# Kernel optimization log

Hardware: AMD Instinct MI355X
Metric: run time of the kernel (lower is better)

The kernel has to match this reference:

```python
import jax, jax.numpy as jnp
import numpy as np

# Module hyperparameters (BNMorph.__init__ defaults + KITTI resolution)
B, H, W = 8, 320, 1024
SEARCH_W = 7      # serachWidth
SEARCH_H = 3      # searchHeight
SPARSITY_RAD = 2
SENSE_R = 20
PIX_DW = 24.0     # pixel_distance_weight
ALPHA_DW = 0.7    # alpha_distance_weight
PIX_MUL_DW = 1.9  # pixel_mulline_distance_weight
ALPHA_PAD = 1.6   # alpha_padding
EDGE_DENSITY = 0.02


def _make_offsets():
    # Exactly mirrors BNMorph.__init__ buffer construction.
    rs = np.arange(-SEARCH_W, SEARCH_W + 1)
    cs = np.arange(-SEARCH_H, SEARCH_H + 1)
    xx, yy = np.meshgrid(rs, cs)
    xx = xx.flatten(); yy = yy.flatten()
    idx = np.argsort(xx ** 2 + yy ** 2)
    xx = xx[idx]; yy = yy[idx]
    ss = np.arange(-SPARSITY_RAD, SPARSITY_RAD + 1)
    sxx, syy = np.meshgrid(ss, ss)
    sxx = sxx.flatten(); syy = syy.flatten()
    cspan = np.arange(-SENSE_R, SENSE_R + 1)
    cxx, cyy = np.meshgrid(cspan, cspan)
    cxx = cxx.flatten(); cyy = cyy.flatten()
    ci = np.argsort(cxx ** 2 + cyy ** 2)
    cxx = cxx[ci]; cyy = cyy[ci]
    f32 = lambda a: jnp.asarray(a, dtype=jnp.float32)
    return f32(xx), f32(yy), f32(sxx), f32(syy), f32(cxx), f32(cyy)


def setup_inputs() -> dict:
    key = jax.random.key(0)
    k1, k2 = jax.random.split(key)
    binMapsrc = (jax.random.uniform(k1, (B, 1, H, W)) < EDGE_DENSITY).astype(jnp.float32)
    binMapdst = (jax.random.uniform(k2, (B, 1, H, W)) < EDGE_DENSITY).astype(jnp.float32)
    xx, yy, sxx, syy, cxx, cyy = _make_offsets()
    return {"binMapsrc": binMapsrc, "binMapdst": binMapdst,
            "xx": xx, "yy": yy, "sxx": sxx, "syy": syy, "cxx": cxx, "cyy": cyy}


def _forward(binMapsrc, binMapdst, xx, yy, sxx, syy, cxx, cyy):
    src = binMapsrc[:, 0] > 0.5  # [B,H,W] bool
    dst = binMapdst[:, 0] > 0.5
    b, h, w = src.shape

    # ---- 1. sparsity filtering of src edge points ----
    # keep an active pixel iff no active pixel precedes it (raster order)
    # inside the sparsity window -> approximates greedy sparsification.
    sdx = sxx.astype(jnp.int32); sdy = syy.astype(jnp.int32)
    prec = ((sdy < 0) | ((sdy == 0) & (sdx < 0))).astype(jnp.float32)
    Ps = jnp.pad(src.astype(jnp.float32),
                 ((0, 0), (SPARSITY_RAD, SPARSITY_RAD), (SPARSITY_RAD, SPARSITY_RAD)))

    def sp_step(acc, off):
        dx, dy, wk = off
        sl = jax.lax.dynamic_slice(Ps, (0, SPARSITY_RAD + dy, SPARSITY_RAD + dx), (b, h, w))
        return acc + sl * wk, None

    acc, _ = jax.lax.scan(sp_step, jnp.zeros((b, h, w), jnp.float32), (sdx, sdy, prec))
    kept = src & (acc < 0.5)

    # ---- 2. windowed nearest-correspondence search in dst ----
    # offsets (xx,yy) are pre-sorted by distance, so the first hit is nearest.
    qdx = xx.astype(jnp.int32); qdy = yy.astype(jnp.int32)
    Pd = jnp.pad(dst, ((0, 0), (SEARCH_H, SEARCH_H), (SEARCH_W, SEARCH_W)))

    def m_step(carry, off):
        found, vx, vy = carry
        dx, dy, dxf, dyf = off
        sl = jax.lax.dynamic_slice(Pd, (0, SEARCH_H + dy, SEARCH_W + dx), (b, h, w))
        hit = sl & kept & (~found)
        vx = jnp.where(hit, dxf, vx)
        vy = jnp.where(hit, dyf, vy)
        return (found | hit, vx, vy), None

    init = (jnp.zeros((b, h, w), bool),
            jnp.zeros((b, h, w), jnp.float32),
            jnp.zeros((b, h, w), jnp.float32))
    (found, vx, vy), _ = jax.lax.scan(m_step, init, (qdx, qdy, xx, yy))

    # ---- 3. distance-weighted morph field (splat = depthwise conv) ----
    d = jnp.sqrt(cxx ** 2 + cyy ** 2)
    wts = ALPHA_DW * jnp.exp(-d * PIX_MUL_DW / PIX_DW)
    R = SENSE_R
    K = jnp.zeros((2 * R + 1, 2 * R + 1), jnp.float32)
    K = K.at[cyy.astype(jnp.int32) + R, cxx.astype(jnp.int32) + R].set(wts)

    m = found.astype(jnp.float32)
    inp = jnp.stack([m, m * vx, m * vy], axis=1)        # [B,3,H,W]
    ker = jnp.tile(K[None, None], (3, 1, 1, 1))          # [3,1,41,41]
    out = jax.lax.conv_general_dilated(
        inp, ker, (1, 1), ((R, R), (R, R)),
        dimension_numbers=("NCHW", "OIHW", "NCHW"), feature_group_count=3)
    den = out[:, 0] + ALPHA_PAD
    dispx = out[:, 1] / den
    dispy = out[:, 2] / den

    ygrid, xgrid = jnp.meshgrid(jnp.arange(h, dtype=jnp.float32),
                                jnp.arange(w, dtype=jnp.float32), indexing="ij")
    morphedx = xgrid + dispx
    morphedy = ygrid + dispy
    orgpts_x = xgrid * m
    orgpts_y = ygrid * m
    correspts_x = (xgrid + vx) * m
    correspts_y = (ygrid + vy) * m
    return morphedx, morphedy, orgpts_x, orgpts_y, correspts_x, correspts_y


def reference(binMapsrc, binMapdst, xx, yy, sxx, syy, cxx, cyy):
    return _forward(binMapsrc, binMapdst, xx, yy, sxx, syy, cxx, cyy)
```

## Files before the change

### kernel.cpp

```cpp
#include <hip/hip_runtime.h>


#define BB 8
#define HH 320
#define WW 1024
#define N_PIX (BB*HH*WW)
#define WPI (HH*(WW/32))
#define RR 20
#define TLW 64
#define TLH 16
#define TXN (WW/TLW)
#define TYN (HH/TLH)
#define NQ 105
#define CAP 160
#define NCR (TLH+40)
#define NSR (NCR+2)
#define NDR (NCR+6)
#define WSTRIDE 49
#define WTABN 2060
#define WTAB_OFF (2*BB*WPI*4)

#define O_WTAB  0
#define O_SRC   8240
#define O_DST   9632
#define O_WAV   8240
#define O_SPT   11120
#define O_PRANK 11792
#define O_SVB   12224
#define O_LCNT  13248
#define SMEM_BYTES 13264

typedef unsigned long long u64;
typedef float v2f __attribute__((ext_vector_type(2)));

__global__ __launch_bounds__(256) void pack_zero(
    const float* __restrict__ src, const float* __restrict__ dst,
    unsigned* __restrict__ packed, float* __restrict__ wtab_g)
{
    int t = threadIdx.x;
    int i = blockIdx.x * 256 + t;
    if (i < WTABN) {
        int row = i / WSTRIDE, c = i - row * WSTRIDE;
        float v = 0.0f;
        if (row <= 40 && c >= 4 && c <= 44) {
            int dxv = c - 24, dyv = row - 20;
            float d = sqrtf((float)(dxv * dxv + dyv * dyv));
            v = 0.7f * expf((-d * 1.9f) / 24.0f);
        }
        wtab_g[i] = v;
    }
    const float4* p = (i < (N_PIX >> 2)) ? (const float4*)src + i
                                         : (const float4*)dst + (i - (N_PIX >> 2));
    float4 v = *p;
    unsigned nib = (v.x > 0.5f ? 1u : 0u) | (v.y > 0.5f ? 2u : 0u)
                 | (v.z > 0.5f ? 4u : 0u) | (v.w > 0.5f ? 8u : 0u);
    unsigned val = nib << ((t & 7) * 4);
    val |= __shfl_xor(val, 1);
    val |= __shfl_xor(val, 2);
    val |= __shfl_xor(val, 4);
    if ((t & 7) == 0) packed[i >> 3] = val;
}

__global__ __launch_bounds__(128, 6) void fused_morph(
    const unsigned* __restrict__ packed,
    const float* __restrict__ xx, const float* __restrict__ yy,
    const float* __restrict__ wtab_g,
    float* __restrict__ out)
{
    __shared__ __align__(16) unsigned char sMem[SMEM_BYTES];
    float* wtab = (float*)(sMem + O_WTAB);
    unsigned (*sSrc)[6] = (unsigned(*)[6])(sMem + O_SRC);
    unsigned (*sDst)[6] = (unsigned(*)[6])(sMem + O_DST);
    unsigned* sPt = (unsigned*)(sMem + O_SPT);
    int* prank = (int*)(sMem + O_PRANK);
    unsigned char* sVB = sMem + O_SVB;
    int* lcnt = (int*)(sMem + O_LCNT);

    int t = threadIdx.x;
    int txT = blockIdx.x, tyT = blockIdx.y, b = blockIdx.z;
    int tx0 = txT * TLW, ty0 = tyT * TLH;
    int wb0 = (tx0 >> 5) - 1;
    const unsigned* psrc = packed + (size_t)b * WPI;
    const unsigned* pdst = packed + (size_t)(BB + b) * WPI;

    for (int i = t; i < WTABN / 4; i += 128)
        ((float4*)wtab)[i] = ((const float4*)wtab_g)[i];
    for (int i = t; i < NSR * 4; i += 128) {
        int r = i >> 2, w = (i & 3) + 1;
        int gy = ty0 - 22 + r, gw = wb0 + (w - 1);
        sSrc[r][w] = (gy >= 0 && gy < HH && gw >= 0 && gw < 32) ? psrc[(gy << 5) + gw] : 0u;
    }
    for (int i = t; i < NDR * 4; i += 128) {
        int r = i >> 2, w = (i & 3) + 1;
        int gy = ty0 - 23 + r, gw = wb0 + (w - 1);
        sDst[r][w] = (gy >= 0 && gy < HH && gw >= 0 && gw < 32) ? pdst[(gy << 5) + gw] : 0u;
    }
    if (t < NDR) { sDst[t][0] = 0; sDst[t][5] = 0; if (t < NSR) { sSrc[t][0] = 0; sSrc[t][5] = 0; } }
    if (t < NQ) {
        int dx = (int)xx[t], dy = (int)yy[t];
        prank[(dy + 3) * 15 + (dx + 7)] = (t << 8) | ((dx + 7) << 4) | (dy + 3);
    }
    ((unsigned*)sVB)[t] = 0; ((unsigned*)sVB)[t + 128] = 0;
    if (t == 0) lcnt[0] = 0;
    __syncthreads();

    for (int task = t; task < NCR * 4; task += 128) {
        int cr = task >> 2, w = (task & 3) + 1;
        unsigned C = sSrc[cr + 2][w];
        unsigned found = 0;
        if (C) {
            #define EXT5(row) ( (u64)((row)[w-1] >> 30) \
                              | ((u64)(row)[w] << 2) \
                              | ((u64)((row)[w+1] & 3u) << 34) )
            u64 a = EXT5(sSrc[cr]) | EXT5(sSrc[cr + 1]);
            u64 or5 = a | (a >> 1) | (a >> 2) | (a >> 3) | (a >> 4);
            u64 e2 = EXT5(sSrc[cr + 2]);
            unsigned kept = C & ~(unsigned)(or5 | e2 | (e2 >> 1));
            if (kept) {
                u64 dil = 0;
                #pragma unroll
                for (int rr = 0; rr < 7; ++rr) {
                    const unsigned* row = sDst[cr + rr];
                    dil |= (u64)(row[w-1] >> 25) | ((u64)row[w] << 7)
                         | ((u64)(row[w+1] & 0x7Fu) << 39);
                }
                u64 a2 = dil | (dil >> 1);
                u64 b2 = a2 | (a2 >> 2);
                u64 c2 = b2 | (b2 >> 4);
                u64 o15 = c2 | (c2 >> 7);
                found = kept & (unsigned)o15;
            }
        }
        if (w == 1) found &= 0xFFFFF000u;
        if (w == 4) found &= 0x000FFFFFu;
        if (found) {
            int nf = __popc(found);
            int base = atomicAdd(lcnt, nf);
            unsigned fi = found;
            while (fi) {
                int bit = __builtin_ctz(fi); fi &= fi - 1;
                int px = tx0 - 32 + ((w - 1) << 5) + bit;
                if (base < CAP) sPt[base] = (unsigned)((cr << 10) | px);
                ++base;
            }
        }
    }
    __syncthreads();
    int nPts = lcnt[0]; if (nPts > CAP) nPts = CAP;

    for (int i = t; i < nPts; i += 128) {
        unsigned e = sPt[i];
        int cr = (int)(e >> 10), px = (int)(e & 1023u);
        int q = px - tx0 + 25;
        int widx = 1 + (q >> 5), sh = q & 31;
        u64 lo = 0, hi = 0;
        #pragma unroll
        for (int rr = 0; rr < 7; ++rr) {
            const unsigned* row = sDst[cr + rr];
            u64 win = (((u64)row[widx] | ((u64)row[widx + 1] << 32)) >> sh) & 0x7FFFull;
            if (rr < 4) lo |= win << (15 * rr);
            else        hi |= win << (15 * (rr - 4));
        }
        int minv = 0x7FFFFFFF;
        while (lo) { int bb2 = __builtin_ctzll(lo); lo &= lo - 1; int rv = prank[bb2];      if (rv < minv) minv = rv; }
        while (hi) { int bb2 = __builtin_ctzll(hi); hi &= hi - 1; int rv = prank[60 + bb2]; if (rv < minv) minv = rv; }
        int vxp7 = (minv >> 4) & 15, vyp3 = minv & 15;
        int py = ty0 - 20 + cr;
        sPt[i] = (unsigned)px | ((unsigned)py << 10)
               | ((unsigned)vxp7 << 19) | ((unsigned)vyp3 << 23);
        if (px >= tx0 && px < tx0 + TLW && cr >= 20 && cr < 20 + TLH)
            sVB[(cr - 20) * TLW + (px - tx0)] =
                (unsigned char)(0x80 | vxp7 | (vyp3 << 4));
    }
    __syncthreads();

    int lane = t & 63, w = __builtin_amdgcn_readfirstlane(t >> 6);
    unsigned* sWavW = (unsigned*)(sMem + O_WAV) + w * 164;
    int wy0 = ty0 + w * 8;
    int cw = 0;
    for (int base = 0; base < nPts; base += 64) {
        int i = base + lane;
        unsigned pk = (i < nPts) ? sPt[i] : 0xFFFFFFFFu;
        int py = (int)((pk >> 10) & 511u);
        bool pass = (i < nPts) & (py >= wy0 - 20) & (py <= wy0 + 27);
        u64 m = __ballot(pass);
        if (pass) {
            int idx = __popcll(m & ((1ull << lane) - 1ull));
            sWavW[cw + idx] = pk;
        }
        cw += __popcll(m);
    }
    int c4 = (cw + 3) & ~3;
    if (lane < c4 - cw) sWavW[cw + lane] = 0xFFFFFFFFu;

    int x0q = tx0 + (lane & 15) * 4;
    int yg  = wy0 + (lane >> 4);

    v2f a0p[2][2] = {};
    v2f av[2][4]  = {};

    for (int p = 0; p < c4; p += 4) {
        uint4 P = *(const uint4*)&sWavW[p];
        #pragma unroll
        for (int k = 0; k < 4; ++k) {
            int spk = __builtin_amdgcn_readfirstlane(
                (int)(k == 0 ? P.x : k == 1 ? P.y : k == 2 ? P.z : P.w));
            int pxp21 = (spk & 1023) + 21;
            int pyp20 = ((spk >> 10) & 511) + 20;
            float pvx = (float)(((spk >> 19) & 15) - 7);
            float pvy = (float)(((spk >> 23) & 7) - 3);
            v2f vv = {pvx, pvy};

            int coff = pxp21 - x0q;
            coff = coff < 0 ? 0 : (coff > 45 ? 45 : coff);
            int d0r = pyp20 - yg;
            #pragma unroll
            for (int ry = 0; ry < 2; ++ry) {
                int dyr = d0r - 4 * ry;
                int rowi = ((unsigned)dyr > 40u) ? 41 : dyr;
                const float* wr = &wtab[rowi * WSTRIDE + coff];
                float w3 = wr[0], w2 = wr[1], w1 = wr[2], w0 = wr[3];
                a0p[ry][0] += (v2f){w0, w1};
                a0p[ry][1] += (v2f){w2, w3};
                av[ry][0] += w0 * vv;
                av[ry][1] += w1 * vv;
                av[ry][2] += w2 * vv;
                av[ry][3] += w3 * vv;
            }
        }
    }

    size_t bbase = (size_t)b * HH * WW;
    int lx = x0q - tx0;
    #pragma unroll
    for (int ry = 0; ry < 2; ++ry) {
        int y = yg + 4 * ry;
        int ly = y - ty0;
        unsigned vb4 = *(const unsigned*)&sVB[ly * TLW + lx];
        size_t idx = bbase + (size_t)y * WW + x0q;
        float d0 = a0p[ry][0].x + 1.6f, d1 = a0p[ry][0].y + 1.6f;
        float d2 = a0p[ry][1].x + 1.6f, d3 = a0p[ry][1].y + 1.6f;
        float4 ox = { (float)x0q     + av[ry][0].x / d0, (float)(x0q+1) + av[ry][1].x / d1,
                      (float)(x0q+2) + av[ry][2].x / d2, (float)(x0q+3) + av[ry][3].x / d3 };
        float4 oy = { (float)y + av[ry][0].y / d0, (float)y + av[ry][1].y / d1,
                      (float)y + av[ry][2].y / d2, (float)y + av[ry][3].y / d3 };
        float4 o2, o3, o4, o5;
        float* po2 = &o2.x; float* po3 = &o3.x; float* po4 = &o4.x; float* po5 = &o5.x;
        #pragma unroll
        for (int jj = 0; jj < 4; ++jj) {
            unsigned by = (vb4 >> (8 * jj)) & 255u;
            float fm  = (float)(by >> 7);
            float fvx = (float)((int)(by & 15u) - 7);
            float fvy = (float)((int)((by >> 4) & 7u) - 3);
            float fx  = (float)(x0q + jj);
            po2[jj] = fx * fm;
            po3[jj] = (float)y * fm;
            po4[jj] = (fx + fvx) * fm;
            po5[jj] = ((float)y + fvy) * fm;
        }
        *reinterpret_cast<float4*>(out + idx)                     = ox;
        *reinterpret_cast<float4*>(out + (size_t)N_PIX + idx)     = oy;
        *reinterpret_cast<float4*>(out + 2 * (size_t)N_PIX + idx) = o2;
        *reinterpret_cast<float4*>(out + 3 * (size_t)N_PIX + idx) = o3;
        *reinterpret_cast<float4*>(out + 4 * (size_t)N_PIX + idx) = o4;
        *reinterpret_cast<float4*>(out + 5 * (size_t)N_PIX + idx) = o5;
    }
}

extern "C" void kernel_launch(void* const* d_in, const int* in_sizes, int n_in,
                              void* d_out, int out_size, void* d_ws, size_t ws_size,
                              hipStream_t stream) {
    const float* src = (const float*)d_in[0];
    const float* dst = (const float*)d_in[1];
    const float* xx  = (const float*)d_in[2];
    const float* yy  = (const float*)d_in[3];
    float* out = (float*)d_out;

    unsigned* packed = (unsigned*)d_ws;
    float*    wtab_g = (float*)((char*)d_ws + WTAB_OFF);

    pack_zero<<<(2 * N_PIX / 4) / 256, 256, 0, stream>>>(src, dst, packed, wtab_g);

    dim3 g2(TXN, TYN, BB);
    fused_morph<<<g2, 128, 0, stream>>>(packed, xx, yy, wtab_g, out);
}
```

Measured before the change: 127.3 us.

## Shrink fused morph tile width to 32 and give each lane one output row

Halves the tile width from 64 to 32 pixels, so the grid doubles and each lane now accumulates a single output row of four pixels instead of two rows. The bit-packed src/dst halo buffers become 5 words per row with new word indexing, and the shared-memory layout, point capacity and weight-table stride are resized to match. The aim is more blocks and fewer registers per thread for better occupancy and load balance. In exchange, halo loading and sparsification/search work are repeated across more tiles, and each wave must rescan the points in its region for fewer outputs.

```diff
diff --git a/kernel.cpp b/kernel.cpp
--- a/kernel.cpp
+++ b/kernel.cpp
@@ -6,29 +6,28 @@
 #define WW 1024
 #define N_PIX (BB*HH*WW)
 #define WPI (HH*(WW/32))
-#define RR 20
-#define TLW 64
+#define TLW 32
 #define TLH 16
 #define TXN (WW/TLW)
 #define TYN (HH/TLH)
 #define NQ 105
-#define CAP 160
+#define CAP 112
 #define NCR (TLH+40)
 #define NSR (NCR+2)
 #define NDR (NCR+6)
-#define WSTRIDE 49
-#define WTABN 2060
+#define WSTRIDE 53
+#define WTABN 2228
 #define WTAB_OFF (2*BB*WPI*4)
 
 #define O_WTAB  0
-#define O_SRC   8240
-#define O_DST   9632
-#define O_WAV   8240
-#define O_SPT   11120
+#define O_SRC   8912
+#define O_WAV   8912
+#define O_DST   10072
+#define O_SPT   11312
 #define O_PRANK 11792
 #define O_SVB   12224
-#define O_LCNT  13248
-#define SMEM_BYTES 13264
+#define O_LCNT  12736
+#define SMEM_BYTES 12752
 
 typedef unsigned long long u64;
 typedef float v2f __attribute__((ext_vector_type(2)));
@@ -69,8 +68,8 @@
 {
     __shared__ __align__(16) unsigned char sMem[SMEM_BYTES];
     float* wtab = (float*)(sMem + O_WTAB);
-    unsigned (*sSrc)[6] = (unsigned(*)[6])(sMem + O_SRC);
-    unsigned (*sDst)[6] = (unsigned(*)[6])(sMem + O_DST);
+    unsigned (*sSrc)[5] = (unsigned(*)[5])(sMem + O_SRC);
+    unsigned (*sDst)[5] = (unsigned(*)[5])(sMem + O_DST);
     unsigned* sPt = (unsigned*)(sMem + O_SPT);
     int* prank = (int*)(sMem + O_PRANK);
     unsigned char* sVB = sMem + O_SVB;
@@ -79,39 +78,37 @@
     int t = threadIdx.x;
     int txT = blockIdx.x, tyT = blockIdx.y, b = blockIdx.z;
     int tx0 = txT * TLW, ty0 = tyT * TLH;
-    int wb0 = (tx0 >> 5) - 1;
     const unsigned* psrc = packed + (size_t)b * WPI;
     const unsigned* pdst = packed + (size_t)(BB + b) * WPI;
 
     for (int i = t; i < WTABN / 4; i += 128)
         ((float4*)wtab)[i] = ((const float4*)wtab_g)[i];
-    for (int i = t; i < NSR * 4; i += 128) {
-        int r = i >> 2, w = (i & 3) + 1;
-        int gy = ty0 - 22 + r, gw = wb0 + (w - 1);
-        sSrc[r][w] = (gy >= 0 && gy < HH && gw >= 0 && gw < 32) ? psrc[(gy << 5) + gw] : 0u;
-    }
-    for (int i = t; i < NDR * 4; i += 128) {
-        int r = i >> 2, w = (i & 3) + 1;
-        int gy = ty0 - 23 + r, gw = wb0 + (w - 1);
-        sDst[r][w] = (gy >= 0 && gy < HH && gw >= 0 && gw < 32) ? pdst[(gy << 5) + gw] : 0u;
-    }
-    if (t < NDR) { sDst[t][0] = 0; sDst[t][5] = 0; if (t < NSR) { sSrc[t][0] = 0; sSrc[t][5] = 0; } }
+    for (int i = t; i < NSR * 5; i += 128) {
+        int r = i / 5, k = i - r * 5;
+        int gy = ty0 - 22 + r, gw = txT - 2 + k;
+        sSrc[r][k] = (gy >= 0 && gy < HH && gw >= 0 && gw < 32) ? psrc[(gy << 5) + gw] : 0u;
+    }
+    for (int i = t; i < NDR * 5; i += 128) {
+        int r = i / 5, k = i - r * 5;
+        int gy = ty0 - 23 + r, gw = txT - 2 + k;
+        sDst[r][k] = (gy >= 0 && gy < HH && gw >= 0 && gw < 32) ? pdst[(gy << 5) + gw] : 0u;
+    }
     if (t < NQ) {
         int dx = (int)xx[t], dy = (int)yy[t];
         prank[(dy + 3) * 15 + (dx + 7)] = (t << 8) | ((dx + 7) << 4) | (dy + 3);
     }
-    ((unsigned*)sVB)[t] = 0; ((unsigned*)sVB)[t + 128] = 0;
+    ((unsigned*)sVB)[t] = 0;
     if (t == 0) lcnt[0] = 0;
     __syncthreads();
 
-    for (int task = t; task < NCR * 4; task += 128) {
-        int cr = task >> 2, w = (task & 3) + 1;
-        unsigned C = sSrc[cr + 2][w];
+    for (int task = t; task < NCR * 3; task += 128) {
+        int cr = task / 3, wd = task - cr * 3 + 1;
+        unsigned C = sSrc[cr + 2][wd];
         unsigned found = 0;
         if (C) {
-            #define EXT5(row) ( (u64)((row)[w-1] >> 30) \
-                              | ((u64)(row)[w] << 2) \
-                              | ((u64)((row)[w+1] & 3u) << 34) )
+            #define EXT5(row) ( (u64)((row)[wd-1] >> 30) \
+                              | ((u64)(row)[wd] << 2) \
+                              | ((u64)((row)[wd+1] & 3u) << 34) )
             u64 a = EXT5(sSrc[cr]) | EXT5(sSrc[cr + 1]);
             u64 or5 = a | (a >> 1) | (a >> 2) | (a >> 3) | (a >> 4);
             u64 e2 = EXT5(sSrc[cr + 2]);
@@ -121,8 +118,8 @@
                 #pragma unroll
                 for (int rr = 0; rr < 7; ++rr) {
                     const unsigned* row = sDst[cr + rr];
-                    dil |= (u64)(row[w-1] >> 25) | ((u64)row[w] << 7)
-                         | ((u64)(row[w+1] & 0x7Fu) << 39);
+                    dil |= (u64)(row[wd-1] >> 25) | ((u64)row[wd] << 7)
+                         | ((u64)(row[wd+1] & 0x7Fu) << 39);
                 }
                 u64 a2 = dil | (dil >> 1);
                 u64 b2 = a2 | (a2 >> 2);
@@ -131,15 +128,15 @@
                 found = kept & (unsigned)o15;
             }
         }
-        if (w == 1) found &= 0xFFFFF000u;
-        if (w == 4) found &= 0x000FFFFFu;
+        if (wd == 1) found &= 0xFFFFF000u;
+        if (wd == 3) found &= 0x000FFFFFu;
         if (found) {
             int nf = __popc(found);
             int base = atomicAdd(lcnt, nf);
             unsigned fi = found;
             while (fi) {
                 int bit = __builtin_ctz(fi); fi &= fi - 1;
-                int px = tx0 - 32 + ((w - 1) << 5) + bit;
+                int px = tx0 - 64 + (wd << 5) + bit;
                 if (base < CAP) sPt[base] = (unsigned)((cr << 10) | px);
                 ++base;
             }
@@ -151,8 +148,8 @@
     for (int i = t; i < nPts; i += 128) {
         unsigned e = sPt[i];
         int cr = (int)(e >> 10), px = (int)(e & 1023u);
-        int q = px - tx0 + 25;
-        int widx = 1 + (q >> 5), sh = q & 31;
+        int q = px - tx0 + 57;
+        int widx = q >> 5, sh = q & 31;
         u64 lo = 0, hi = 0;
         #pragma unroll
         for (int rr = 0; rr < 7; ++rr) {
@@ -175,7 +172,7 @@
     __syncthreads();
 
     int lane = t & 63, w = __builtin_amdgcn_readfirstlane(t >> 6);
-    unsigned* sWavW = (unsigned*)(sMem + O_WAV) + w * 164;
+    unsigned* sWavW = (unsigned*)(sMem + O_WAV) + w * 120;
     int wy0 = ty0 + w * 8;
     int cw = 0;
     for (int base = 0; base < nPts; base += 64) {
@@ -193,11 +190,11 @@
     int c4 = (cw + 3) & ~3;
     if (lane < c4 - cw) sWavW[cw + lane] = 0xFFFFFFFFu;
 
-    int x0q = tx0 + (lane & 15) * 4;
-    int yg  = wy0 + (lane >> 4);
-
-    v2f a0p[2][2] = {};
-    v2f av[2][4]  = {};
+    int x0q = tx0 + (lane & 7) * 4;
+    int y   = wy0 + (lane >> 3);
+
+    v2f a0p0 = {}, a0p1 = {};
+    v2f av[4] = {};
 
     for (int p = 0; p < c4; p += 4) {
         uint4 P = *(const uint4*)&sWavW[p];
@@ -205,66 +202,56 @@
         for (int k = 0; k < 4; ++k) {
             int spk = __builtin_amdgcn_readfirstlane(
                 (int)(k == 0 ? P.x : k == 1 ? P.y : k == 2 ? P.z : P.w));
-            int pxp21 = (spk & 1023) + 21;
+            int px = spk & 1023;
             int pyp20 = ((spk >> 10) & 511) + 20;
             float pvx = (float)(((spk >> 19) & 15) - 7);
             float pvy = (float)(((spk >> 23) & 7) - 3);
             v2f vv = {pvx, pvy};
 
-            int coff = pxp21 - x0q;
+            int coff = px + 21 - x0q;
             coff = coff < 0 ? 0 : (coff > 45 ? 45 : coff);
-            int d0r = pyp20 - yg;
-            #pragma unroll
-            for (int ry = 0; ry < 2; ++ry) {
-                int dyr = d0r - 4 * ry;
-                int rowi = ((unsigned)dyr > 40u) ? 41 : dyr;
-                const float* wr = &wtab[rowi * WSTRIDE + coff];
-                float w3 = wr[0], w2 = wr[1], w1 = wr[2], w0 = wr[3];
-                a0p[ry][0] += (v2f){w0, w1};
-                a0p[ry][1] += (v2f){w2, w3};
-                av[ry][0] += w0 * vv;
-                av[ry][1] += w1 * vv;
-                av[ry][2] += w2 * vv;
-                av[ry][3] += w3 * vv;
-            }
+            int dyr = pyp20 - y;
+            int rowi = ((unsigned)dyr > 40u) ? 41 : dyr;
+            const float* wr = &wtab[rowi * WSTRIDE + coff];
+            float w3 = wr[0], w2 = wr[1], w1 = wr[2], w0 = wr[3];
+            a0p0 += (v2f){w0, w1};
+            a0p1 += (v2f){w2, w3};
+            av[0] += w0 * vv;
+            av[1] += w1 * vv;
+            av[2] += w2 * vv;
+            av[3] += w3 * vv;
         }
     }
 
     size_t bbase = (size_t)b * HH * WW;
-    int lx = x0q - tx0;
+    unsigned vb4 = *(const unsigned*)&sVB[(y - ty0) * TLW + (x0q - tx0)];
+    size_t idx = bbase + (size_t)y * WW + x0q;
+    float d0 = a0p0.x + 1.6f, d1 = a0p0.y + 1.6f;
+    float d2 = a0p1.x + 1.6f, d3 = a0p1.y + 1.6f;
+    float4 ox = { (float)x0q     + av[0].x / d0, (float)(x0q+1) + av[1].x / d1,
+                  (float)(x0q+2) + av[2].x / d2, (float)(x0q+3) + av[3].x / d3 };
+    float4 oy = { (float)y + av[0].y / d0, (float)y + av[1].y / d1,
+                  (float)y + av[2].y / d2, (float)y + av[3].y / d3 };
+    float4 o2, o3, o4, o5;
+    float* po2 = &o2.x; float* po3 = &o3.x; float* po4 = &o4.x; float* po5 = &o5.x;
     #pragma unroll
-    for (int ry = 0; ry < 2; ++ry) {
-        int y = yg + 4 * ry;
-        int ly = y - ty0;
-        unsigned vb4 = *(const unsigned*)&sVB[ly * TLW + lx];
-        size_t idx = bbase + (size_t)y * WW + x0q;
-        float d0 = a0p[ry][0].x + 1.6f, d1 = a0p[ry][0].y + 1.6f;
-        float d2 = a0p[ry][1].x + 1.6f, d3 = a0p[ry][1].y + 1.6f;
-        float4 ox = { (float)x0q     + av[ry][0].x / d0, (float)(x0q+1) + av[ry][1].x / d1,
-                      (float)(x0q+2) + av[ry][2].x / d2, (float)(x0q+3) + av[ry][3].x / d3 };
-        float4 oy = { (float)y + av[ry][0].y / d0, (float)y + av[ry][1].y / d1,
-                      (float)y + av[ry][2].y / d2, (float)y + av[ry][3].y / d3 };
-        float4 o2, o3, o4, o5;
-        float* po2 = &o2.x; float* po3 = &o3.x; float* po4 = &o4.x; float* po5 = &o5.x;
-        #pragma unroll
-        for (int jj = 0; jj < 4; ++jj) {
-            unsigned by = (vb4 >> (8 * jj)) & 255u;
-            float fm  = (float)(by >> 7);
-            float fvx = (float)((int)(by & 15u) - 7);
-            float fvy = (float)((int)((by >> 4) & 7u) - 3);
-            float fx  = (float)(x0q + jj);
-            po2[jj] = fx * fm;
-            po3[jj] = (float)y * fm;
-            po4[jj] = (fx + fvx) * fm;
-            po5[jj] = ((float)y + fvy) * fm;
-        }
-        *reinterpret_cast<float4*>(out + idx)                     = ox;
-        *reinterpret_cast<float4*>(out + (size_t)N_PIX + idx)     = oy;
-        *reinterpret_cast<float4*>(out + 2 * (size_t)N_PIX + idx) = o2;
-        *reinterpret_cast<float4*>(out + 3 * (size_t)N_PIX + idx) = o3;
-        *reinterpret_cast<float4*>(out + 4 * (size_t)N_PIX + idx) = o4;
-        *reinterpret_cast<float4*>(out + 5 * (size_t)N_PIX + idx) = o5;
-    }
+    for (int jj = 0; jj < 4; ++jj) {
+        unsigned by = (vb4 >> (8 * jj)) & 255u;
+        float fm  = (float)(by >> 7);
+        float fvx = (float)((int)(by & 15u) - 7);
+        float fvy = (float)((int)((by >> 4) & 7u) - 3);
+        float fx  = (float)(x0q + jj);
+        po2[jj] = fx * fm;
+        po3[jj] = (float)y * fm;
+        po4[jj] = (fx + fvx) * fm;
+        po5[jj] = ((float)y + fvy) * fm;
+    }
+    *reinterpret_cast<float4*>(out + idx)                     = ox;
+    *reinterpret_cast<float4*>(out + (size_t)N_PIX + idx)     = oy;
+    *reinterpret_cast<float4*>(out + 2 * (size_t)N_PIX + idx) = o2;
+    *reinterpret_cast<float4*>(out + 3 * (size_t)N_PIX + idx) = o3;
+    *reinterpret_cast<float4*>(out + 4 * (size_t)N_PIX + idx) = o4;
+    *reinterpret_cast<float4*>(out + 5 * (size_t)N_PIX + idx) = o5;
 }
 
 extern "C" void kernel_launch(void* const* d_in, const int* in_sizes, int n_in,
```

New measurement: 126.3 us. About the same (-0.8%).
